# Optimization experiments

Measured on AMD Instinct MI355X. Metric: run time of the kernel, lower is better.

Reference implementation:

```python
import jax, jax.numpy as jnp
import numpy as np

EPS = 1e-6
H = 8        # num_heads
DH = 64      # head dim = embed_dim // num_heads
LN_EPS = 1e-5


def _layernorm(x, g, b):
    m = jnp.mean(x, axis=-1, keepdims=True)
    v = jnp.mean(jnp.square(x - m), axis=-1, keepdims=True)
    return (x - m) / jnp.sqrt(v + LN_EPS) * g + b


def _flow_attention(x, Wq, bq, Wk, bk, Wv, bv, Wo, bo):
    # Non-causal Flow-Attention (Flowformer): kernelized sigmoid Q/K,
    # flow-conservation sink/source normalization, linear-attention kv trick.
    B, L, D = x.shape
    S = L
    q = jax.nn.sigmoid((x @ Wq + bq).reshape(B, L, H, DH).transpose(0, 2, 1, 3))  # bhld
    k = jax.nn.sigmoid((x @ Wk + bk).reshape(B, S, H, DH).transpose(0, 2, 1, 3))
    v = (x @ Wv + bv).reshape(B, S, H, DH).transpose(0, 2, 1, 3)

    sink_incoming = 1.0 / jnp.einsum('nhld,nhd->nhl', q + EPS, k.sum(axis=2) + EPS)
    source_outgoing = 1.0 / jnp.einsum('nhld,nhd->nhl', k + EPS, q.sum(axis=2) + EPS)
    conserved_sink = jnp.einsum('nhld,nhd->nhl', q + EPS,
                                (k * source_outgoing[..., None]).sum(axis=2) + EPS)
    conserved_source = jnp.einsum('nhld,nhd->nhl', k + EPS,
                                  (q * sink_incoming[..., None]).sum(axis=2) + EPS)
    conserved_source = jnp.clip(conserved_source, -1.0, 1.0)
    sink_allocation = jax.nn.sigmoid(conserved_sink * (float(L) / float(S)))
    source_competition = jax.nn.softmax(conserved_source, axis=-1) * float(S)

    # linear attention: kv = k^T (v * comp), out = (q * sink_in) kv
    kv = jnp.einsum('nhld,nhlm->nhdm', k, v * source_competition[..., None])
    o = jnp.einsum('nhld,nhdm->nhlm', q * sink_incoming[..., None], kv)
    o = o * sink_allocation[..., None]
    o = o.transpose(0, 2, 1, 3).reshape(B, L, D)
    return o @ Wo + bo


def setup_inputs() -> dict:
    key = jax.random.key(0)
    ks = jax.random.split(key, 16)
    B, L, D, F = 2, 16384, 512, 2048
    s = 0.02
    inp = {
        'x': jax.random.normal(ks[0], (B, L, D), dtype=jnp.float32),
        'Wq': jax.random.normal(ks[1], (D, D), dtype=jnp.float32) * s,
        'bq': jnp.zeros((D,), jnp.float32),
        'Wk': jax.random.normal(ks[2], (D, D), dtype=jnp.float32) * s,
        'bk': jnp.zeros((D,), jnp.float32),
        'Wv': jax.random.normal(ks[3], (D, D), dtype=jnp.float32) * s,
        'bv': jnp.zeros((D,), jnp.float32),
        'Wo': jax.random.normal(ks[4], (D, D), dtype=jnp.float32) * s,
        'bo': jnp.zeros((D,), jnp.float32),
        'W1': jax.random.normal(ks[5], (D, F), dtype=jnp.float32) * s,
        'b1': jnp.zeros((F,), jnp.float32),
        'W2': jax.random.normal(ks[6], (F, D), dtype=jnp.float32) * s,
        'b2': jnp.zeros((D,), jnp.float32),
        'g1': jnp.ones((D,), jnp.float32),
        'be1': jnp.zeros((D,), jnp.float32),
        'g2': jnp.ones((D,), jnp.float32),
        'be2': jnp.zeros((D,), jnp.float32),
    }
    return inp


def reference(x, Wq, bq, Wk, bk, Wv, bv, Wo, bo, W1, b1, W2, b2, g1, be1, g2, be2):
    # norm_first FlowformerLayer. NOTE: original _sa_block returns
    # dropout(attn(x))[0, :, :] -> [L, D], broadcast-added over batch (faithful).
    sa = _flow_attention(_layernorm(x, g1, be1), Wq, bq, Wk, bk, Wv, bv, Wo, bo)[0]
    x = x + sa  # [B,L,D] + [L,D]
    h = _layernorm(x, g2, be2)
    h = jax.nn.gelu(h @ W1 + b1, approximate=False) @ W2 + b2
    return x + h
```

## Files before the change

kernel.cpp:

```cpp
#include <hip/hip_runtime.h>
#include <hip/hip_bf16.h>
#include <cstdint>
#include <cstddef>


#define L_SEQ 16384
#define EPSF 1e-6f

typedef __bf16 b16x8 __attribute__((ext_vector_type(8)));
typedef __bf16 b16x4 __attribute__((ext_vector_type(4)));
typedef float  f32x4 __attribute__((ext_vector_type(4)));

#define FENCE() asm volatile("" ::: "memory")
#define BARF()  { FENCE(); __builtin_amdgcn_s_barrier(); FENCE(); }
#define WAITV(n) asm volatile("s_waitcnt vmcnt(" #n ")" ::: "memory")

__device__ __forceinline__ void gload16(const void* g, void* l) {
  __builtin_amdgcn_global_load_lds((const __attribute__((address_space(1))) void*)g,
                                   (__attribute__((address_space(3))) void*)l, 16, 0, 0);
}

__device__ __forceinline__ float sigmoidf_(float x) { return 1.f / (1.f + __expf(-x)); }

__global__ __launch_bounds__(256) void convT(const float* __restrict__ src,
                                             __bf16* __restrict__ dst, int K, int N) {
  __shared__ float tile[32][33];
  const int k0 = blockIdx.y * 32, n0 = blockIdx.x * 32;
  const int tx = threadIdx.x & 31, ty = threadIdx.x >> 5;
#pragma unroll
  for (int i = 0; i < 32; i += 8) tile[ty + i][tx] = src[(size_t)(k0 + ty + i) * N + n0 + tx];
  __syncthreads();
#pragma unroll
  for (int i = 0; i < 32; i += 8)
    dst[(size_t)(n0 + ty + i) * K + k0 + tx] = (__bf16)tile[tx][ty + i];
}

__global__ __launch_bounds__(256) void biascat_k(const float* __restrict__ bq,
                                                 const float* __restrict__ bk,
                                                 const float* __restrict__ bv,
                                                 float* __restrict__ bc) {
  int i = blockIdx.x * 256 + threadIdx.x;
  bc[i] = (i < 512) ? bq[i] : (i < 1024) ? bk[i - 512] : bv[i - 1024];
}

__global__ __launch_bounds__(256) void zero_k(float* __restrict__ p, int n) {
  int i = blockIdx.x * 256 + threadIdx.x;
  if (i < n) p[i] = 0.f;
}

__global__ __launch_bounds__(128) void ln_rows(const float* __restrict__ x,
                                               const float* __restrict__ g,
                                               const float* __restrict__ be,
                                               __bf16* __restrict__ out) {
  const int row = blockIdx.x, t = threadIdx.x;
  const float4 xv = reinterpret_cast<const float4*>(x + (size_t)row * 512)[t];
  float s = xv.x + xv.y + xv.z + xv.w;
  float s2 = xv.x * xv.x + xv.y * xv.y + xv.z * xv.z + xv.w * xv.w;
#pragma unroll
  for (int off = 32; off > 0; off >>= 1) { s += __shfl_down(s, off); s2 += __shfl_down(s2, off); }
  __shared__ float red[4];
  if ((t & 63) == 0) { red[(t >> 6) * 2] = s; red[(t >> 6) * 2 + 1] = s2; }
  __syncthreads();
  const float S = red[0] + red[2], S2 = red[1] + red[3];
  const float mean = S * (1.f / 512.f);
  const float var = S2 * (1.f / 512.f) - mean * mean;
  const float inv = rsqrtf(var + 1e-5f);
  const float4 gv = reinterpret_cast<const float4*>(g)[t];
  const float4 bv = reinterpret_cast<const float4*>(be)[t];
  b16x4 o;
  o[0] = (__bf16)((xv.x - mean) * inv * gv.x + bv.x);
  o[1] = (__bf16)((xv.y - mean) * inv * gv.y + bv.y);
  o[2] = (__bf16)((xv.z - mean) * inv * gv.z + bv.z);
  o[3] = (__bf16)((xv.w - mean) * inv * gv.w + bv.w);
  reinterpret_cast<b16x4*>(out + (size_t)row * 512)[t] = o;
}

__global__ __launch_bounds__(128) void x2ln2_k(const float* __restrict__ x,
                                               const float* __restrict__ sa0,
                                               const float* __restrict__ sa1,
                                               const float* __restrict__ bo,
                                               const float* __restrict__ g,
                                               const float* __restrict__ be,
                                               float* __restrict__ xout,
                                               __bf16* __restrict__ lnout) {
  const int row = blockIdx.x, t = threadIdx.x;
  const int l = row & (L_SEQ - 1);
  float4 xv = reinterpret_cast<const float4*>(x + (size_t)row * 512)[t];
  const float4 s0 = reinterpret_cast<const float4*>(sa0 + (size_t)l * 512)[t];
  const float4 s1 = reinterpret_cast<const float4*>(sa1 + (size_t)l * 512)[t];
  const float4 bb = reinterpret_cast<const float4*>(bo)[t];
  xv.x += s0.x + s1.x + bb.x; xv.y += s0.y + s1.y + bb.y;
  xv.z += s0.z + s1.z + bb.z; xv.w += s0.w + s1.w + bb.w;
  reinterpret_cast<float4*>(xout + (size_t)row * 512)[t] = xv;
  float s = xv.x + xv.y + xv.z + xv.w;
  float s2 = xv.x * xv.x + xv.y * xv.y + xv.z * xv.z + xv.w * xv.w;
#pragma unroll
  for (int off = 32; off > 0; off >>= 1) { s += __shfl_down(s, off); s2 += __shfl_down(s2, off); }
  __shared__ float red[4];
  if ((t & 63) == 0) { red[(t >> 6) * 2] = s; red[(t >> 6) * 2 + 1] = s2; }
  __syncthreads();
  const float S = red[0] + red[2], S2 = red[1] + red[3];
  const float mean = S * (1.f / 512.f);
  const float var = S2 * (1.f / 512.f) - mean * mean;
  const float inv = rsqrtf(var + 1e-5f);
  const float4 gv = reinterpret_cast<const float4*>(g)[t];
  const float4 bv = reinterpret_cast<const float4*>(be)[t];
  b16x4 o;
  o[0] = (__bf16)((xv.x - mean) * inv * gv.x + bv.x);
  o[1] = (__bf16)((xv.y - mean) * inv * gv.y + bv.y);
  o[2] = (__bf16)((xv.z - mean) * inv * gv.z + bv.z);
  o[3] = (__bf16)((xv.w - mean) * inv * gv.w + bv.w);
  reinterpret_cast<b16x4*>(lnout + (size_t)row * 512)[t] = o;
}

#define DSA(mh, ks)                                                           \
  {                                                                           \
    const int ab = bsel * 16384 + (wr * 128 + (mh) * 64 + fr) * 64;           \
    const int sw = ((((ks) << 2) | kb) ^ l7) << 3;                            \
    av[0] = *reinterpret_cast<const b16x8*>(&lds[ab + sw]);                   \
    av[1] = *reinterpret_cast<const b16x8*>(&lds[ab + 1024 + sw]);            \
    av[2] = *reinterpret_cast<const b16x8*>(&lds[ab + 2048 + sw]);            \
    av[3] = *reinterpret_cast<const b16x8*>(&lds[ab + 3072 + sw]);            \
  }
#define DSB(ks)                                                               \
  {                                                                           \
    const int bb = 32768 + bsel * 16384 + (wc * 64 + fr) * 64;                \
    const int sw = ((((ks) << 2) | kb) ^ l7) << 3;                            \
    bv[0] = *reinterpret_cast<const b16x8*>(&lds[bb + sw]);                   \
    bv[1] = *reinterpret_cast<const b16x8*>(&lds[bb + 1024 + sw]);            \
    bv[2] = *reinterpret_cast<const b16x8*>(&lds[bb + 2048 + sw]);            \
    bv[3] = *reinterpret_cast<const b16x8*>(&lds[bb + 3072 + sw]);            \
  }
#define MM(mh)                                                                \
  __builtin_amdgcn_s_setprio(1);                                              \
  _Pragma("unroll") for (int m = 0; m < 4; m++)                               \
      _Pragma("unroll") for (int n = 0; n < 4; n++) acc[(mh) * 4 + m][n] =    \
      __builtin_amdgcn_mfma_f32_16x16x32_bf16(av[m], bv[n],                   \
                                              acc[(mh) * 4 + m][n], 0, 0, 0); \
  __builtin_amdgcn_s_setprio(0);

template <int EPI, int KSPL>
__global__ __launch_bounds__(512) void gemm256(const __bf16* __restrict__ A,
                                               const __bf16* __restrict__ Bt,
                                               const int M, const int N, const int K,
                                               const float* __restrict__ bias,
                                               float* __restrict__ f0,
                                               __bf16* __restrict__ h0,
                                               __bf16* __restrict__ h1,
                                               float* __restrict__ f1,
                                               float* __restrict__ f2) {
  __shared__ alignas(16) __bf16 lds[65536];

  if constexpr (KSPL) {
    const int z = blockIdx.y;
    A += (size_t)z * (K >> 1);
    Bt += (size_t)z * (K >> 1);
    f0 += (size_t)z * ((size_t)M * N);
  }
  const int nt = KSPL ? (K >> 7) : (K >> 6);

  const int nwg = gridDim.x;
  const int orig = blockIdx.x;
  const int cpx = nwg >> 3;
  const int wg = (orig & 7) * cpx + (orig >> 3);
  const int gx = N >> 8;
  const int bm = (wg / gx) << 8;
  const int bn = (wg % gx) << 8;

  const int t = threadIdx.x;
  const int w = t >> 6, lane = t & 63;
  const int wr = w >> 2, wc = w & 3;
  const int lr = lane >> 3;
  const int sx = (lane & 7) ^ lr;
  const int fr = lane & 15;
  const int kb = lane >> 4;
  const int l7 = lane & 7;

  const __bf16* As = A + (size_t)(bm + w * 8 + lr) * K + sx * 8;
  const __bf16* Bs = Bt + (size_t)(bn + w * 8 + lr) * K + sx * 8;

  f32x4 acc[8][4] = {};

  auto STG_A = [&](int s, int j0, int j1) {
    const __bf16* ap = As + (s << 6);
    const int dbase = (s & 1) * 16384 + (w << 9);
    gload16(ap + (size_t)(j0 << 6) * K, &lds[dbase + (j0 << 12)]);
    gload16(ap + (size_t)(j1 << 6) * K, &lds[dbase + (j1 << 12)]);
  };
  auto STG_B = [&](int s, int j0, int j1) {
    const __bf16* bp = Bs + (s << 6);
    const int dbase = 32768 + (s & 1) * 16384 + (w << 9);
    gload16(bp + (size_t)(j0 << 6) * K, &lds[dbase + (j0 << 12)]);
    gload16(bp + (size_t)(j1 << 6) * K, &lds[dbase + (j1 << 12)]);
  };

  STG_A(0, 0, 2);
  STG_B(0, 0, 1);
  STG_B(0, 2, 3);
  STG_A(0, 1, 3);
  STG_A(1, 0, 2);
  WAITV(2);
  BARF();

  for (int s = 0; s < nt; s++) {
    const int bsel = s & 1;
    b16x8 av[4], bv[4];
    DSA(0, 0);
    DSB(0);
    if (s + 1 < nt) { STG_B(s + 1, 0, 1); WAITV(4); } else { WAITV(0); }
    BARF();
    MM(0);
    BARF();
    DSA(1, 0);
    if (s + 1 < nt) STG_B(s + 1, 2, 3);
    BARF();
    MM(1);
    BARF();
    DSA(0, 1);
    DSB(1);
    if (s + 1 < nt) STG_A(s + 1, 1, 3);
    BARF();
    MM(0);
    BARF();
    DSA(1, 1);
    if (s + 2 < nt) { STG_A(s + 2, 0, 2); WAITV(4); }
    else if (s + 1 < nt) { WAITV(2); }
    BARF();
    MM(1);
    BARF();
  }

  const int r0 = kb * 4;
  const int cc = fr;
  if constexpr (EPI == 0) {
    const int which = bn >> 9;
    float cs[4] = {0.f, 0.f, 0.f, 0.f};
#pragma unroll
    for (int m = 0; m < 8; m++) {
#pragma unroll
      for (int n = 0; n < 4; n++) {
        const int col = bn + wc * 64 + n * 16 + cc;
        const int c2 = col & 511;
#pragma unroll
        for (int r = 0; r < 4; r++) {
          const int row = bm + wr * 128 + m * 16 + r0 + r;
          float val = acc[m][n][r] + bias[col];
          if (which < 2) {
            val = sigmoidf_(val);
            cs[n] += val;
            ((which == 0) ? h0 : h1)[(size_t)row * 512 + c2] = (__bf16)val;
          } else {
            f0[(size_t)row * 512 + c2] = val;
          }
        }
      }
    }
    if (which < 2) {
      float* sums = (which == 0) ? f1 : f2;
#pragma unroll
      for (int n = 0; n < 4; n++) {
        float s = cs[n];
        s += __shfl_xor(s, 16);
        s += __shfl_xor(s, 32);
        if (kb == 0) atomicAdd(&sums[(bn & 511) + wc * 64 + n * 16 + cc], s);
      }
    }
  } else {
#pragma unroll
    for (int m = 0; m < 8; m++) {
#pragma unroll
      for (int n = 0; n < 4; n++) {
        const int col = bn + wc * 64 + n * 16 + cc;
#pragma unroll
        for (int r = 0; r < 4; r++) {
          const int row = bm + wr * 128 + m * 16 + r0 + r;
          float val = acc[m][n][r];
          if constexpr (EPI == 1) {
            f0[(size_t)row * N + col] = val;
          } else if constexpr (EPI == 2) {
            const float xg = val + bias[col];
            const float gel = 0.5f * xg * (1.f + erff(xg * 0.70710678118f));
            h0[(size_t)row * N + col] = (__bf16)gel;
          } else {
            const size_t idx = (size_t)row * N + col;
            f0[idx] = f0[idx] + val + bias[col];
          }
        }
      }
    }
  }
}

__global__ __launch_bounds__(256) void attn_pass1(const __bf16* __restrict__ q,
                                                  const __bf16* __restrict__ k,
                                                  const float* __restrict__ qsum,
                                                  const float* __restrict__ ksum,
                                                  float* __restrict__ si_out,
                                                  float* __restrict__ qkpart) {
  __shared__ float lsQ[512], lsK[512];
  const int t = threadIdx.x, lane = t & 63, wv = t >> 6;
  const int c0 = lane * 8;
  lsQ[t] = 0.f; lsQ[t + 256] = 0.f;
  lsK[t] = 0.f; lsK[t + 256] = 0.f;
  __syncthreads();
  float qs[8], ks[8];
#pragma unroll
  for (int j = 0; j < 8; j++) {
    qs[j] = qsum[c0 + j] + EPSF;
    ks[j] = ksum[c0 + j] + EPSF;
  }
  const int h = lane >> 3;
  float qacc[8] = {}, kacc[8] = {};
#pragma unroll 1
  for (int i = 0; i < 8; i++) {
    const int l = blockIdx.x * 32 + wv * 8 + i;
    const b16x8 q8 = *reinterpret_cast<const b16x8*>(q + (size_t)l * 512 + c0);
    const b16x8 k8 = *reinterpret_cast<const b16x8*>(k + (size_t)l * 512 + c0);
    float qf[8], kf[8];
    float p1 = 0.f, p2 = 0.f;
#pragma unroll
    for (int j = 0; j < 8; j++) {
      qf[j] = (float)q8[j]; kf[j] = (float)k8[j];
      p1 += (qf[j] + EPSF) * ks[j];
      p2 += (kf[j] + EPSF) * qs[j];
    }
    p1 += __shfl_xor(p1, 1); p2 += __shfl_xor(p2, 1);
    p1 += __shfl_xor(p1, 2); p2 += __shfl_xor(p2, 2);
    p1 += __shfl_xor(p1, 4); p2 += __shfl_xor(p2, 4);
    const float siv = 1.f / p1, sov = 1.f / p2;
    if ((lane & 7) == 0) si_out[h * L_SEQ + l] = siv;
#pragma unroll
    for (int j = 0; j < 8; j++) { qacc[j] += qf[j] * siv; kacc[j] += kf[j] * sov; }
  }
#pragma unroll
  for (int j = 0; j < 8; j++) {
    atomicAdd(&lsQ[c0 + j], qacc[j]);
    atomicAdd(&lsK[c0 + j], kacc[j]);
  }
  __syncthreads();
  float* qp = qkpart + (size_t)blockIdx.x * 1024;
  qp[t] = lsQ[t];
  qp[t + 256] = lsQ[t + 256];
  qp[t + 512] = lsK[t];
  qp[t + 768] = lsK[t + 256];
}

__global__ __launch_bounds__(256) void reduce_qk(const float* __restrict__ qkpart,
                                                 float* __restrict__ outv) {
  const int i = blockIdx.x * 256 + threadIdx.x;
  float s = 0.f;
#pragma unroll 4
  for (int b = 0; b < 512; b++) s += qkpart[(size_t)b * 1024 + i];
  outv[i] = s;
}

__global__ __launch_bounds__(256) void kv_part(const __bf16* __restrict__ k,
                                               const float* __restrict__ v,
                                               const float* __restrict__ qsi,
                                               float* __restrict__ kvpart,
                                               float* __restrict__ separt) {
  const int h = blockIdx.y, bx = blockIdx.x, t = threadIdx.x;
  __shared__ float lsK[64 * 68];
  __shared__ float lsV[64 * 68];
  __shared__ float lsRed[256];
  const int r = t >> 2, cq = (t & 3) * 16;
  float qv[16];
#pragma unroll
  for (int j = 0; j < 16; j++) qv[j] = qsi[h * 64 + cq + j] + EPSF;
  const int d = t & 63, mg = t >> 6;
  f32x4 acc4[4] = {};
  float seloc = 0.f;
#pragma unroll 1
  for (int sc = 0; sc < 4; sc++) {
    const int l = bx * 256 + sc * 64 + r;
    __syncthreads();
    const b16x8 k8a = *reinterpret_cast<const b16x8*>(k + (size_t)l * 512 + h * 64 + cq);
    const b16x8 k8b = *reinterpret_cast<const b16x8*>(k + (size_t)l * 512 + h * 64 + cq + 8);
    f32x4 v4[4];
#pragma unroll
    for (int jj = 0; jj < 4; jj++)
      v4[jj] = *reinterpret_cast<const f32x4*>(v + (size_t)l * 512 + h * 64 + cq + jj * 4);
    float kf[16];
#pragma unroll
    for (int j = 0; j < 8; j++) { kf[j] = (float)k8a[j]; kf[8 + j] = (float)k8b[j]; }
    float p = 0.f;
#pragma unroll
    for (int j = 0; j < 16; j++) p += (kf[j] + EPSF) * qv[j];
    p += __shfl_xor(p, 1);
    p += __shfl_xor(p, 2);
    p = fminf(fmaxf(p, -1.f), 1.f);
    const float ce = __expf(p);
    if ((t & 3) == 0) seloc += ce;
#pragma unroll
    for (int j = 0; j < 16; j++) lsK[r * 68 + cq + j] = kf[j];
#pragma unroll
    for (int jj = 0; jj < 4; jj++)
      *reinterpret_cast<f32x4*>(&lsV[r * 68 + cq + jj * 4]) = v4[jj] * ce;
    __syncthreads();
    for (int rr = 0; rr < 64; rr++) {
      const float kd = lsK[rr * 68 + d];
      const f32x4* lv = reinterpret_cast<const f32x4*>(&lsV[rr * 68 + mg * 16]);
#pragma unroll
      for (int jj = 0; jj < 4; jj++) acc4[jj] += lv[jj] * kd;
    }
  }
  float* kp = kvpart + ((size_t)h * 64 + bx) * 4096;
#pragma unroll
  for (int jj = 0; jj < 4; jj++)
    *reinterpret_cast<f32x4*>(&kp[d * 64 + mg * 16 + jj * 4]) = acc4[jj];
  lsRed[t] = ((t & 3) == 0) ? seloc : 0.f;
  __syncthreads();
  for (int s2 = 128; s2 > 0; s2 >>= 1) {
    if (t < s2) lsRed[t] += lsRed[t + s2];
    __syncthreads();
  }
  if (t == 0) separt[h * 64 + bx] = lsRed[0];
}

__global__ __launch_bounds__(256) void kv_reduce(const float* __restrict__ kvpart,
                                                 const float* __restrict__ separt,
                                                 float* __restrict__ kvout,
                                                 float* __restrict__ sumexp) {
  const int h = blockIdx.y, t = threadIdx.x;
  const int i = blockIdx.x * 256 + t;
  float s = 0.f;
#pragma unroll 4
  for (int b = 0; b < 64; b++) s += kvpart[((size_t)h * 64 + b) * 4096 + i];
  kvout[h * 4096 + i] = s;
  if (blockIdx.x == 0 && t < 64) {
    float e = separt[h * 64 + t];
#pragma unroll
    for (int off2 = 32; off2 > 0; off2 >>= 1) e += __shfl_down(e, off2);
    if (t == 0) sumexp[h] = e;
  }
}

__global__ __launch_bounds__(256) void o_kernel(const __bf16* __restrict__ q,
                                                const float* __restrict__ kvin,
                                                const float* __restrict__ si,
                                                const float* __restrict__ kso,
                                                const float* __restrict__ sumexp,
                                                __bf16* __restrict__ o) {
  const int h = blockIdx.y;
  const int l0 = blockIdx.x * 32;
  const int t = threadIdx.x;
  __shared__ float lsKV[64 * 64];
  __shared__ float lsQ[32 * 65];
  __shared__ float lsF[32];
  const float Sfac = (float)L_SEQ / sumexp[h];
#pragma unroll
  for (int j = 0; j < 16; j++) lsKV[t + j * 256] = kvin[h * 4096 + t + j * 256];
  const int r = t >> 3, c8 = (t & 7) * 8;
  float ksov[8];
#pragma unroll
  for (int j = 0; j < 8; j++) ksov[j] = kso[h * 64 + c8 + j] + EPSF;
  const b16x8 q8 = *reinterpret_cast<const b16x8*>(q + (size_t)(l0 + r) * 512 + h * 64 + c8);
  float p = 0.f;
#pragma unroll
  for (int j = 0; j < 8; j++) {
    const float qf = (float)q8[j];
    lsQ[r * 65 + c8 + j] = qf;
    p += (qf + EPSF) * ksov[j];
  }
  p += __shfl_xor(p, 1);
  p += __shfl_xor(p, 2);
  p += __shfl_xor(p, 4);
  if ((t & 7) == 0) lsF[r] = sigmoidf_(p) * si[h * L_SEQ + l0 + r] * Sfac;
  __syncthreads();
  const int m = t & 63, rg = t >> 6;
#pragma unroll 1
  for (int i = 0; i < 8; i++) {
    const int rr = rg + i * 4;
    float a = 0.f;
#pragma unroll
    for (int dd = 0; dd < 64; dd++) a += lsQ[rr * 65 + dd] * lsKV[dd * 64 + m];
    o[(size_t)(l0 + rr) * 512 + h * 64 + m] = (__bf16)(a * lsF[rr]);
  }
}

extern "C" void kernel_launch(void* const* d_in, const int* in_sizes, int n_in,
                              void* d_out, int out_size, void* d_ws, size_t ws_size,
                              hipStream_t stream) {
  const float* x  = (const float*)d_in[0];
  const float* Wq = (const float*)d_in[1];
  const float* bq = (const float*)d_in[2];
  const float* Wk = (const float*)d_in[3];
  const float* bk = (const float*)d_in[4];
  const float* Wv = (const float*)d_in[5];
  const float* bv = (const float*)d_in[6];
  const float* Wo = (const float*)d_in[7];
  const float* bo = (const float*)d_in[8];
  const float* W1 = (const float*)d_in[9];
  const float* b1 = (const float*)d_in[10];
  const float* W2 = (const float*)d_in[11];
  const float* b2 = (const float*)d_in[12];
  const float* g1 = (const float*)d_in[13];
  const float* be1 = (const float*)d_in[14];
  const float* g2 = (const float*)d_in[15];
  const float* be2 = (const float*)d_in[16];
  float* out = (float*)d_out;

  char* ws = (char*)d_ws;
  size_t off = 0;
  auto alloc = [&](size_t bytes) -> char* {
    char* p = ws + off;
    off += (bytes + 255) & ~(size_t)255;
    return p;
  };

  char* regA = alloc(134217728);
  __bf16* ln1  = (__bf16*)regA;
  __bf16* qb16 = (__bf16*)(regA + 16777216);
  __bf16* kb16 = (__bf16*)(regA + 33554432);
  float*  vb   = (float*)(regA + 50331648);
  __bf16* ob   = (__bf16*)(regA + 83886080);
  float*  sa   = (float*)regA;
  __bf16* act  = (__bf16*)regA;

  __bf16* ln2 = (__bf16*)alloc((size_t)32768 * 512 * 2);
  __bf16* Wqkvt = (__bf16*)alloc((size_t)1536 * 512 * 2);
  __bf16* Wot = (__bf16*)alloc((size_t)512 * 512 * 2);
  __bf16* W1t = (__bf16*)alloc((size_t)2048 * 512 * 2);
  __bf16* W2t = (__bf16*)alloc((size_t)512 * 2048 * 2);
  float* biascat = (float*)alloc(1536 * 4);
  float* si = (float*)alloc((size_t)8 * L_SEQ * 4);
  float* stats = (float*)alloc(34880 * 4);
  float* qsum = stats;
  float* ksum = stats + 512;
  float* qsi = stats + 1024;
  float* kso = stats + 1536;
  float* sumexp = stats + 2048;
  float* kvbuf = stats + 2112;
  float* kvpart = (float*)alloc((size_t)8 * 64 * 4096 * 4);
  float* separt = (float*)alloc(512 * 4);
  float* qkpart = (float*)alloc((size_t)512 * 1024 * 4);

  convT<<<dim3(16, 16), 256, 0, stream>>>(Wq, Wqkvt, 512, 512);
  convT<<<dim3(16, 16), 256, 0, stream>>>(Wk, Wqkvt + (size_t)512 * 512, 512, 512);
  convT<<<dim3(16, 16), 256, 0, stream>>>(Wv, Wqkvt + (size_t)1024 * 512, 512, 512);
  convT<<<dim3(16, 16), 256, 0, stream>>>(Wo, Wot, 512, 512);
  convT<<<dim3(64, 16), 256, 0, stream>>>(W1, W1t, 512, 2048);
  convT<<<dim3(16, 64), 256, 0, stream>>>(W2, W2t, 2048, 512);
  biascat_k<<<6, 256, 0, stream>>>(bq, bk, bv, biascat);
  zero_k<<<(2112 + 255) / 256, 256, 0, stream>>>(stats, 2112);

  ln_rows<<<L_SEQ, 128, 0, stream>>>(x, g1, be1, ln1);
  gemm256<0, 0><<<384, 512, 0, stream>>>(ln1, Wqkvt, L_SEQ, 1536, 512,
                                         biascat, vb, qb16, kb16, qsum, ksum);

  attn_pass1<<<512, 256, 0, stream>>>(qb16, kb16, qsum, ksum, si, qkpart);
  reduce_qk<<<4, 256, 0, stream>>>(qkpart, qsi);
  kv_part<<<dim3(64, 8), 256, 0, stream>>>(kb16, vb, qsi, kvpart, separt);
  kv_reduce<<<dim3(16, 8), 256, 0, stream>>>(kvpart, separt, kvbuf, sumexp);
  o_kernel<<<dim3(L_SEQ / 32, 8), 256, 0, stream>>>(qb16, kvbuf, si, kso, sumexp, ob);

  gemm256<1, 1><<<dim3(128, 2), 512, 0, stream>>>(ob, Wot, L_SEQ, 512, 512,
                                                  nullptr, sa, nullptr, nullptr,
                                                  nullptr, nullptr);

  x2ln2_k<<<2 * L_SEQ, 128, 0, stream>>>(x, sa, sa + (size_t)L_SEQ * 512, bo,
                                         g2, be2, out, ln2);

  gemm256<2, 0><<<1024, 512, 0, stream>>>(ln2, W1t, 2 * L_SEQ, 2048, 512,
                                          b1, nullptr, act, nullptr, nullptr, nullptr);
  gemm256<3, 0><<<256, 512, 0, stream>>>(act, W2t, 2 * L_SEQ, 512, 2048,
                                         b2, out, nullptr, nullptr, nullptr, nullptr);
}
```

Baseline: 549.1 us.

## Replace 256x256 pipelined GEMM with simpler 128x128 tile GEMM

Swaps the 256x256-tile, 512-thread GEMM with fine-grained interleaved staging for a 128x128-tile, 256-thread kernel with K-step 32 and simple double buffering. The aim is more workgroups and higher occupancy (launch bounds allow 4 blocks per CU) with less LDS per block. In exchange it drops the XOR swizzle on LDS reads, waits for all loads each iteration, and halves per-tile data reuse, which may add bank conflicts and memory traffic.

```diff
diff --git a/kernel.cpp b/kernel.cpp
--- a/kernel.cpp
+++ b/kernel.cpp
@@ -113,43 +113,17 @@
   reinterpret_cast<b16x4*>(lnout + (size_t)row * 512)[t] = o;
 }
 
-#define DSA(mh, ks)                                                           \
-  {                                                                           \
-    const int ab = bsel * 16384 + (wr * 128 + (mh) * 64 + fr) * 64;           \
-    const int sw = ((((ks) << 2) | kb) ^ l7) << 3;                            \
-    av[0] = *reinterpret_cast<const b16x8*>(&lds[ab + sw]);                   \
-    av[1] = *reinterpret_cast<const b16x8*>(&lds[ab + 1024 + sw]);            \
-    av[2] = *reinterpret_cast<const b16x8*>(&lds[ab + 2048 + sw]);            \
-    av[3] = *reinterpret_cast<const b16x8*>(&lds[ab + 3072 + sw]);            \
-  }
-#define DSB(ks)                                                               \
-  {                                                                           \
-    const int bb = 32768 + bsel * 16384 + (wc * 64 + fr) * 64;                \
-    const int sw = ((((ks) << 2) | kb) ^ l7) << 3;                            \
-    bv[0] = *reinterpret_cast<const b16x8*>(&lds[bb + sw]);                   \
-    bv[1] = *reinterpret_cast<const b16x8*>(&lds[bb + 1024 + sw]);            \
-    bv[2] = *reinterpret_cast<const b16x8*>(&lds[bb + 2048 + sw]);            \
-    bv[3] = *reinterpret_cast<const b16x8*>(&lds[bb + 3072 + sw]);            \
-  }
-#define MM(mh)                                                                \
-  __builtin_amdgcn_s_setprio(1);                                              \
-  _Pragma("unroll") for (int m = 0; m < 4; m++)                               \
-      _Pragma("unroll") for (int n = 0; n < 4; n++) acc[(mh) * 4 + m][n] =    \
-      __builtin_amdgcn_mfma_f32_16x16x32_bf16(av[m], bv[n],                   \
-                                              acc[(mh) * 4 + m][n], 0, 0, 0); \
-  __builtin_amdgcn_s_setprio(0);
-
 template <int EPI, int KSPL>
-__global__ __launch_bounds__(512) void gemm256(const __bf16* __restrict__ A,
-                                               const __bf16* __restrict__ Bt,
-                                               const int M, const int N, const int K,
-                                               const float* __restrict__ bias,
-                                               float* __restrict__ f0,
-                                               __bf16* __restrict__ h0,
-                                               __bf16* __restrict__ h1,
-                                               float* __restrict__ f1,
-                                               float* __restrict__ f2) {
-  __shared__ alignas(16) __bf16 lds[65536];
+__global__ __launch_bounds__(256, 4) void gemm128(const __bf16* __restrict__ A,
+                                                  const __bf16* __restrict__ Bt,
+                                                  const int M, const int N, const int K,
+                                                  const float* __restrict__ bias,
+                                                  float* __restrict__ f0,
+                                                  __bf16* __restrict__ h0,
+                                                  __bf16* __restrict__ h1,
+                                                  float* __restrict__ f1,
+                                                  float* __restrict__ f2) {
+  __shared__ alignas(16) __bf16 lds[16384];
 
   if constexpr (KSPL) {
     const int z = blockIdx.y;
@@ -157,76 +131,58 @@
     Bt += (size_t)z * (K >> 1);
     f0 += (size_t)z * ((size_t)M * N);
   }
-  const int nt = KSPL ? (K >> 7) : (K >> 6);
+  const int nt = KSPL ? (K >> 6) : (K >> 5);
 
   const int nwg = gridDim.x;
   const int orig = blockIdx.x;
   const int cpx = nwg >> 3;
   const int wg = (orig & 7) * cpx + (orig >> 3);
-  const int gx = N >> 8;
-  const int bm = (wg / gx) << 8;
-  const int bn = (wg % gx) << 8;
+  const int gx = N >> 7;
+  const int bm = (wg / gx) << 7;
+  const int bn = (wg % gx) << 7;
 
   const int t = threadIdx.x;
   const int w = t >> 6, lane = t & 63;
-  const int wr = w >> 2, wc = w & 3;
-  const int lr = lane >> 3;
-  const int sx = (lane & 7) ^ lr;
+  const int wr = w >> 1, wc = w & 1;
   const int fr = lane & 15;
   const int kb = lane >> 4;
-  const int l7 = lane & 7;
-
-  const __bf16* As = A + (size_t)(bm + w * 8 + lr) * K + sx * 8;
-  const __bf16* Bs = Bt + (size_t)(bn + w * 8 + lr) * K + sx * 8;
-
-  f32x4 acc[8][4] = {};
-
-  auto STG_A = [&](int s, int j0, int j1) {
-    const __bf16* ap = As + (s << 6);
-    const int dbase = (s & 1) * 16384 + (w << 9);
-    gload16(ap + (size_t)(j0 << 6) * K, &lds[dbase + (j0 << 12)]);
-    gload16(ap + (size_t)(j1 << 6) * K, &lds[dbase + (j1 << 12)]);
+
+  const __bf16* As = A + (size_t)(bm + (t >> 2)) * K + (t & 3) * 8;
+  const __bf16* Bs = Bt + (size_t)(bn + (t >> 2)) * K + (t & 3) * 8;
+
+  f32x4 acc[4][4] = {};
+
+  auto STG = [&](int s) {
+    const int sel = (s & 1) * 4096;
+    const __bf16* ap = As + (s << 5);
+    const __bf16* bp = Bs + (s << 5);
+    gload16(ap, &lds[sel + t * 8]);
+    gload16(ap + (size_t)64 * K, &lds[sel + 2048 + t * 8]);
+    gload16(bp, &lds[8192 + sel + t * 8]);
+    gload16(bp + (size_t)64 * K, &lds[8192 + sel + 2048 + t * 8]);
   };
-  auto STG_B = [&](int s, int j0, int j1) {
-    const __bf16* bp = Bs + (s << 6);
-    const int dbase = 32768 + (s & 1) * 16384 + (w << 9);
-    gload16(bp + (size_t)(j0 << 6) * K, &lds[dbase + (j0 << 12)]);
-    gload16(bp + (size_t)(j1 << 6) * K, &lds[dbase + (j1 << 12)]);
-  };
-
-  STG_A(0, 0, 2);
-  STG_B(0, 0, 1);
-  STG_B(0, 2, 3);
-  STG_A(0, 1, 3);
-  STG_A(1, 0, 2);
-  WAITV(2);
+
+  STG(0);
+  WAITV(0);
   BARF();
 
   for (int s = 0; s < nt; s++) {
-    const int bsel = s & 1;
+    if (s + 1 < nt) STG(s + 1);
+    const int ab = (s & 1) * 4096 + (wr * 64 + fr) * 32 + kb * 8;
+    const int bb2 = 8192 + (s & 1) * 4096 + (wc * 64 + fr) * 32 + kb * 8;
     b16x8 av[4], bv[4];
-    DSA(0, 0);
-    DSB(0);
-    if (s + 1 < nt) { STG_B(s + 1, 0, 1); WAITV(4); } else { WAITV(0); }
-    BARF();
-    MM(0);
-    BARF();
-    DSA(1, 0);
-    if (s + 1 < nt) STG_B(s + 1, 2, 3);
-    BARF();
-    MM(1);
-    BARF();
-    DSA(0, 1);
-    DSB(1);
-    if (s + 1 < nt) STG_A(s + 1, 1, 3);
-    BARF();
-    MM(0);
-    BARF();
-    DSA(1, 1);
-    if (s + 2 < nt) { STG_A(s + 2, 0, 2); WAITV(4); }
-    else if (s + 1 < nt) { WAITV(2); }
-    BARF();
-    MM(1);
+#pragma unroll
+    for (int m = 0; m < 4; m++)
+      av[m] = *reinterpret_cast<const b16x8*>(&lds[ab + m * 512]);
+#pragma unroll
+    for (int n = 0; n < 4; n++)
+      bv[n] = *reinterpret_cast<const b16x8*>(&lds[bb2 + n * 512]);
+#pragma unroll
+    for (int m = 0; m < 4; m++)
+#pragma unroll
+      for (int n = 0; n < 4; n++)
+        acc[m][n] = __builtin_amdgcn_mfma_f32_16x16x32_bf16(av[m], bv[n], acc[m][n], 0, 0, 0);
+    WAITV(0);
     BARF();
   }
 
@@ -236,14 +192,14 @@
     const int which = bn >> 9;
     float cs[4] = {0.f, 0.f, 0.f, 0.f};
 #pragma unroll
-    for (int m = 0; m < 8; m++) {
+    for (int m = 0; m < 4; m++) {
 #pragma unroll
       for (int n = 0; n < 4; n++) {
         const int col = bn + wc * 64 + n * 16 + cc;
         const int c2 = col & 511;
 #pragma unroll
         for (int r = 0; r < 4; r++) {
-          const int row = bm + wr * 128 + m * 16 + r0 + r;
+          const int row = bm + wr * 64 + m * 16 + r0 + r;
           float val = acc[m][n][r] + bias[col];
           if (which < 2) {
             val = sigmoidf_(val);
@@ -267,13 +223,13 @@
     }
   } else {
 #pragma unroll
-    for (int m = 0; m < 8; m++) {
+    for (int m = 0; m < 4; m++) {
 #pragma unroll
       for (int n = 0; n < 4; n++) {
         const int col = bn + wc * 64 + n * 16 + cc;
 #pragma unroll
         for (int r = 0; r < 4; r++) {
-          const int row = bm + wr * 128 + m * 16 + r0 + r;
+          const int row = bm + wr * 64 + m * 16 + r0 + r;
           float val = acc[m][n][r];
           if constexpr (EPI == 1) {
             f0[(size_t)row * N + col] = val;
@@ -545,8 +501,8 @@
   zero_k<<<(2112 + 255) / 256, 256, 0, stream>>>(stats, 2112);
 
   ln_rows<<<L_SEQ, 128, 0, stream>>>(x, g1, be1, ln1);
-  gemm256<0, 0><<<384, 512, 0, stream>>>(ln1, Wqkvt, L_SEQ, 1536, 512,
-                                         biascat, vb, qb16, kb16, qsum, ksum);
+  gemm128<0, 0><<<1536, 256, 0, stream>>>(ln1, Wqkvt, L_SEQ, 1536, 512,
+                                          biascat, vb, qb16, kb16, qsum, ksum);
 
   attn_pass1<<<512, 256, 0, stream>>>(qb16, kb16, qsum, ksum, si, qkpart);
   reduce_qk<<<4, 256, 0, stream>>>(qkpart, qsi);
@@ -554,15 +510,15 @@
   kv_reduce<<<dim3(16, 8), 256, 0, stream>>>(kvpart, separt, kvbuf, sumexp);
   o_kernel<<<dim3(L_SEQ / 32, 8), 256, 0, stream>>>(qb16, kvbuf, si, kso, sumexp, ob);
 
-  gemm256<1, 1><<<dim3(128, 2), 512, 0, stream>>>(ob, Wot, L_SEQ, 512, 512,
+  gemm128<1, 1><<<dim3(512, 2), 256, 0, stream>>>(ob, Wot, L_SEQ, 512, 512,
                                                   nullptr, sa, nullptr, nullptr,
                                                   nullptr, nullptr);
 
   x2ln2_k<<<2 * L_SEQ, 128, 0, stream>>>(x, sa, sa + (size_t)L_SEQ * 512, bo,
                                          g2, be2, out, ln2);
 
-  gemm256<2, 0><<<1024, 512, 0, stream>>>(ln2, W1t, 2 * L_SEQ, 2048, 512,
+  gemm128<2, 0><<<4096, 256, 0, stream>>>(ln2, W1t, 2 * L_SEQ, 2048, 512,
                                           b1, nullptr, act, nullptr, nullptr, nullptr);
-  gemm256<3, 0><<<256, 512, 0, stream>>>(act, W2t, 2 * L_SEQ, 512, 2048,
-                                         b2, out, nullptr, nullptr, nullptr, nullptr);
-}
+  gemm128<3, 0><<<1024, 256, 0, stream>>>(act, W2t, 2 * L_SEQ, 512, 2048,
+                                          b2, out, nullptr, nullptr, nullptr, nullptr);
+}
```

Result: faster. 514.0 us (-6.4%).
